# Kernel optimization log

Measured on AMD Instinct MI355X. Metric: run time of the kernel, lower is better.

Reference implementation:

```python
import jax, jax.numpy as jnp
import numpy as np

EPS = 0.1
SHAPE = (1, 1, 96, 96)  # [B, C, H, W]


def setup_inputs() -> dict:
    key = jax.random.key(0)
    x = jax.random.normal(key, SHAPE, dtype=jnp.float32)
    return {"x": x}


def reference(x):
    eps = EPS
    B, C, H, W = x.shape
    N = C * H * W  # max possible new error terms; buffer grows to 1 + N slots

    # clip the eps-ball into [0, 1]: bias shifts, error radius shrinks
    r_low = jax.nn.relu(eps - x) * 0.5
    r_high = jax.nn.relu(x - (1.0 - eps)) * 0.5
    bias = x + r_low - r_high                  # zonotope center, [B,C,H,W]
    err = eps - r_low - r_high                 # per-pixel error magnitude

    ef = err.reshape(N)
    cond = ef >= 0                             # which pixels get an error term
    # stream compaction: k-th true condition -> error-term slot 1+k (slot 0 = bias)
    slot = jnp.cumsum(cond.astype(jnp.int32))  # 1-based compacted index
    err_idx = jnp.where(cond, slot, N + 1)     # out-of-range -> dropped

    f, i, j = jnp.unravel_index(jnp.arange(N), (C, H, W))

    zono = jnp.zeros((B, 1 + N, C, H, W), dtype=x.dtype)
    zono = zono.at[0, 0].set(bias[0])
    zono = zono.at[0, err_idx, f, i, j].set(ef, mode='drop')
    return zono
```

## Files before the change

### kernel.cpp

```cpp
#include <hip/hip_runtime.h>

#define NPIX 9216
#define NROWS (NPIX + 1)
#define ROW4 (NPIX / 4)
#define EPSV 0.1f

typedef float f32x4 __attribute__((ext_vector_type(4)));

__global__ __launch_bounds__(1024) void prep_kernel(const float* __restrict__ x,
                                                    int* __restrict__ inv) {
    __shared__ int wsum[16];
    const int tid  = threadIdx.x;
    const int lane = tid & 63;
    const int wid  = tid >> 6;

    for (int s = tid; s < NROWS; s += 1024) inv[s] = -1;

    const int PER  = NPIX / 1024;
    const int base = tid * PER;

    int c_loc[PER];
    int cnt = 0;
#pragma unroll
    for (int k = 0; k < PER; ++k) {
        const float xv     = x[base + k];
        const float r_low  = fmaxf(EPSV - xv, 0.0f) * 0.5f;
        const float r_high = fmaxf(xv - (1.0f - EPSV), 0.0f) * 0.5f;
        const float e      = EPSV - r_low - r_high;
        c_loc[k] = (e >= 0.0f) ? 1 : 0;
        cnt += c_loc[k];
    }

    int v = cnt;
#pragma unroll
    for (int off = 1; off < 64; off <<= 1) {
        const int t = __shfl_up(v, off, 64);
        if (lane >= off) v += t;
    }
    if (lane == 63) wsum[wid] = v;
    __syncthreads();

    int woff = 0;
#pragma unroll
    for (int w = 0; w < 16; ++w) woff += (w < wid) ? wsum[w] : 0;

    int slot = woff + v - cnt;
#pragma unroll
    for (int k = 0; k < PER; ++k) {
        if (c_loc[k]) {
            ++slot;
            inv[slot] = base + k;
        }
    }
}

__global__ __launch_bounds__(256) void write_kernel(const float* __restrict__ x,
                                                    const int* __restrict__ inv,
                                                    f32x4* __restrict__ out) {
    const int row = blockIdx.x;
    const int tid = threadIdx.x;
    f32x4* orow = out + (long long)row * ROW4;

    if (row == 0) {
        const f32x4* x4 = reinterpret_cast<const f32x4*>(x);
#pragma unroll
        for (int it = 0; it < 9; ++it) {
            const int c4 = tid + it * 256;
            const f32x4 xv = x4[c4];
            f32x4 o;
#pragma unroll
            for (int d = 0; d < 4; ++d) {
                const float v = xv[d];
                o[d] = v + fmaxf(EPSV - v, 0.0f) * 0.5f
                         - fmaxf(v - (1.0f - EPSV), 0.0f) * 0.5f;
            }
            __builtin_nontemporal_store(o, &orow[c4]);
        }
    } else {
        const int p  = inv[row];
        const int pp = (p >= 0) ? p : 0;
        const float xv     = x[pp];
        const float r_low  = fmaxf(EPSV - xv, 0.0f) * 0.5f;
        const float r_high = fmaxf(xv - (1.0f - EPSV), 0.0f) * 0.5f;
        const float e      = EPSV - r_low - r_high;
#pragma unroll
        for (int it = 0; it < 9; ++it) {
            const int c4 = tid + it * 256;
            const int c0 = c4 * 4;
            f32x4 o;
            o.x = (p == c0)     ? e : 0.0f;
            o.y = (p == c0 + 1) ? e : 0.0f;
            o.z = (p == c0 + 2) ? e : 0.0f;
            o.w = (p == c0 + 3) ? e : 0.0f;
            __builtin_nontemporal_store(o, &orow[c4]);
        }
    }
}

extern "C" void kernel_launch(void* const* d_in, const int* in_sizes, int n_in,
                              void* d_out, int out_size, void* d_ws, size_t ws_size,
                              hipStream_t stream) {
    const float* x = (const float*)d_in[0];
    float* out = (float*)d_out;

    int* inv = (int*)d_ws;

    prep_kernel<<<1, 1024, 0, stream>>>(x, inv);
    write_kernel<<<NROWS, 256, 0, stream>>>(x, inv, (f32x4*)out);
}
```

Measured before the change: 73.06 us.

## Zero-fill error rows with a bulk kernel, then scatter diagonal entries directly

Replaces the slot-inverse map and per-row compare-and-write kernel with two kernels. A wide kernel writes zeros to all error-term rows, then a single-block kernel does the compaction scan, stores each error value straight into its compacted row and writes the bias row. This removes the workspace index array, the per-row gather of x and the select logic. The trade-off is that the single-block scatter of about 9216 strided stores now runs after the bulk fill, in series, instead of before it.

```diff
diff --git a/kernel.cpp b/kernel.cpp
--- a/kernel.cpp
+++ b/kernel.cpp
@@ -7,26 +7,35 @@
 
 typedef float f32x4 __attribute__((ext_vector_type(4)));
 
-__global__ __launch_bounds__(1024) void prep_kernel(const float* __restrict__ x,
-                                                    int* __restrict__ inv) {
+__global__ __launch_bounds__(256) void fill_kernel(f32x4* __restrict__ out) {
+    const int tid = blockIdx.x * 256 + threadIdx.x;
+    const f32x4 z = {0.0f, 0.0f, 0.0f, 0.0f};
+    f32x4* p = out + ROW4 + tid;
+#pragma unroll 9
+    for (int it = 0; it < 81; ++it) {
+        __builtin_nontemporal_store(z, p);
+        p += 262144;
+    }
+}
+
+__global__ __launch_bounds__(1024) void finish_kernel(const float* __restrict__ x,
+                                                      float* __restrict__ out) {
     __shared__ int wsum[16];
     const int tid  = threadIdx.x;
     const int lane = tid & 63;
     const int wid  = tid >> 6;
+    const int base = tid * 9;
 
-    for (int s = tid; s < NROWS; s += 1024) inv[s] = -1;
-
-    const int PER  = NPIX / 1024;
-    const int base = tid * PER;
-
-    int c_loc[PER];
-    int cnt = 0;
+    float e_loc[9];
+    int   c_loc[9];
+    int   cnt = 0;
 #pragma unroll
-    for (int k = 0; k < PER; ++k) {
+    for (int k = 0; k < 9; ++k) {
         const float xv     = x[base + k];
         const float r_low  = fmaxf(EPSV - xv, 0.0f) * 0.5f;
         const float r_high = fmaxf(xv - (1.0f - EPSV), 0.0f) * 0.5f;
         const float e      = EPSV - r_low - r_high;
+        e_loc[k] = e;
         c_loc[k] = (e >= 0.0f) ? 1 : 0;
         cnt += c_loc[k];
     }
@@ -46,53 +55,28 @@
 
     int slot = woff + v - cnt;
 #pragma unroll
-    for (int k = 0; k < PER; ++k) {
+    for (int k = 0; k < 9; ++k) {
         if (c_loc[k]) {
             ++slot;
-            inv[slot] = base + k;
+            out[(long long)slot * NPIX + (base + k)] = e_loc[k];
         }
     }
-}
 
-__global__ __launch_bounds__(256) void write_kernel(const float* __restrict__ x,
-                                                    const int* __restrict__ inv,
-                                                    f32x4* __restrict__ out) {
-    const int row = blockIdx.x;
-    const int tid = threadIdx.x;
-    f32x4* orow = out + (long long)row * ROW4;
-
-    if (row == 0) {
-        const f32x4* x4 = reinterpret_cast<const f32x4*>(x);
+    const f32x4* x4 = reinterpret_cast<const f32x4*>(x);
+    f32x4* o4 = reinterpret_cast<f32x4*>(out);
 #pragma unroll
-        for (int it = 0; it < 9; ++it) {
-            const int c4 = tid + it * 256;
+    for (int it = 0; it < 3; ++it) {
+        const int c4 = tid + it * 1024;
+        if (c4 < ROW4) {
             const f32x4 xv = x4[c4];
             f32x4 o;
 #pragma unroll
             for (int d = 0; d < 4; ++d) {
-                const float v = xv[d];
-                o[d] = v + fmaxf(EPSV - v, 0.0f) * 0.5f
-                         - fmaxf(v - (1.0f - EPSV), 0.0f) * 0.5f;
+                const float vv = xv[d];
+                o[d] = vv + fmaxf(EPSV - vv, 0.0f) * 0.5f
+                          - fmaxf(vv - (1.0f - EPSV), 0.0f) * 0.5f;
             }
-            __builtin_nontemporal_store(o, &orow[c4]);
-        }
-    } else {
-        const int p  = inv[row];
-        const int pp = (p >= 0) ? p : 0;
-        const float xv     = x[pp];
-        const float r_low  = fmaxf(EPSV - xv, 0.0f) * 0.5f;
-        const float r_high = fmaxf(xv - (1.0f - EPSV), 0.0f) * 0.5f;
-        const float e      = EPSV - r_low - r_high;
-#pragma unroll
-        for (int it = 0; it < 9; ++it) {
-            const int c4 = tid + it * 256;
-            const int c0 = c4 * 4;
-            f32x4 o;
-            o.x = (p == c0)     ? e : 0.0f;
-            o.y = (p == c0 + 1) ? e : 0.0f;
-            o.z = (p == c0 + 2) ? e : 0.0f;
-            o.w = (p == c0 + 3) ? e : 0.0f;
-            __builtin_nontemporal_store(o, &orow[c4]);
+            o4[c4] = o;
         }
     }
 }
@@ -103,8 +87,6 @@
     const float* x = (const float*)d_in[0];
     float* out = (float*)d_out;
 
-    int* inv = (int*)d_ws;
-
-    prep_kernel<<<1, 1024, 0, stream>>>(x, inv);
-    write_kernel<<<NROWS, 256, 0, stream>>>(x, inv, (f32x4*)out);
+    fill_kernel<<<1024, 256, 0, stream>>>((f32x4*)out);
+    finish_kernel<<<1, 1024, 0, stream>>>(x, out);
 }
```

Result: no change. 73.88 us (+1.1%).
